# Kernel tuning notes

Hardware: AMD Instinct MI355X
Metric: run time of the kernel (lower is better)

Reference implementation:

```python
import jax, jax.numpy as jnp
import numpy as np

N_NODES = 100000
N_EDGES = 300000
N_TYPES = 3
HID = 128
EMB = 64
N_GRAPHS = 4096
T_STEPS = 4


def setup_inputs() -> dict:
    key = jax.random.key(0)
    ks = jax.random.split(key, 12)
    s = 1.0 / np.sqrt(HID)
    return {
        "node_features": jax.random.normal(ks[0], (N_NODES, HID), jnp.float32),
        "edge_index": jax.random.randint(ks[1], (N_TYPES, 2, N_EDGES), 0, N_NODES),
        "node_to_graph_id": jnp.sort(jax.random.randint(ks[2], (N_NODES,), 0, N_GRAPHS)),
        "W_msg": jax.random.normal(ks[3], (N_TYPES, HID, HID), jnp.float32) * s,
        "b_msg": jnp.zeros((N_TYPES, HID), jnp.float32),
        "W_ih": jax.random.normal(ks[4], (3 * HID, HID), jnp.float32) * s,
        "W_hh": jax.random.normal(ks[5], (3 * HID, HID), jnp.float32) * s,
        "b_ih": jnp.zeros((3 * HID,), jnp.float32),
        "b_hh": jnp.zeros((3 * HID,), jnp.float32),
        "W_proj": jax.random.normal(ks[6], (EMB, HID), jnp.float32) * s,
        "b_proj": jnp.zeros((EMB,), jnp.float32),
        "W_gate": jax.random.normal(ks[7], (EMB, HID), jnp.float32) * s,
        "b_gate": jnp.zeros((EMB,), jnp.float32),
    }


def _gru_cell(m, h, W_ih, W_hh, b_ih, b_hh):
    # torch.nn.GRUCell math; gates ordered (r, z, n)
    gi = m @ W_ih.T + b_ih          # [N, 3H]
    gh = h @ W_hh.T + b_hh          # [N, 3H]
    i_r, i_z, i_n = jnp.split(gi, 3, axis=-1)
    h_r, h_z, h_n = jnp.split(gh, 3, axis=-1)
    r = jax.nn.sigmoid(i_r + h_r)
    z = jax.nn.sigmoid(i_z + h_z)
    n = jnp.tanh(i_n + r * h_n)
    return (1.0 - z) * n + z * h


def reference(node_features, edge_index, node_to_graph_id,
              W_msg, b_msg, W_ih, W_hh, b_ih, b_hh,
              W_proj, b_proj, W_gate, b_gate):
    h = node_features  # [N, H]

    def per_type(eidx, W, b, h):
        src, dst = eidx[0], eidx[1]
        m = h[src] @ W + b  # gather + per-edge-type linear, [E, H]
        return jax.ops.segment_sum(m, dst, num_segments=N_NODES)

    for _ in range(T_STEPS):  # fixed small T: python loop is fine
        msgs = jax.vmap(per_type, in_axes=(0, 0, 0, None))(edge_index, W_msg, b_msg, h)
        m = msgs.sum(axis=0)  # [N, H] aggregated over edge types
        h = _gru_cell(m, h, W_ih, W_hh, b_ih, b_hh)

    # gated index_add graph readout (mlp_down is identity)
    proj = h @ W_proj.T + b_proj                 # [N, E]
    gate = jax.nn.sigmoid(h @ W_gate.T + b_gate)  # [N, E]
    graph_feats = jax.ops.segment_sum(gate * proj, node_to_graph_id,
                                      num_segments=N_GRAPHS)
    return graph_feats
```

## Files before the change

kernel.cpp:

```cpp
#include <hip/hip_runtime.h>
#include <hip/hip_bf16.h>
#include <math.h>

#define NN 100000
#define NNP 100096
#define NE 300000
#define HID 128
#define EMB 64
#define NG 4096
#define DEG_CAP 32
#define XS 512

typedef __bf16 bf16x8 __attribute__((ext_vector_type(8)));
typedef float  f32x16 __attribute__((ext_vector_type(16)));
typedef short  short8 __attribute__((ext_vector_type(8)));

typedef const __attribute__((address_space(1))) unsigned int* gas_u32;
typedef __attribute__((address_space(3))) unsigned int* las_u32;

__device__ __forceinline__ void gload16(const void* g, void* l) {
    __builtin_amdgcn_global_load_lds((gas_u32)g, (las_u32)l, 16, 0, 0);
}

__device__ __forceinline__ float bf2f(unsigned short u) {
    unsigned int x = ((unsigned int)u) << 16;
    return __builtin_bit_cast(float, x);
}
__device__ __forceinline__ unsigned short f2bf(float f) {
    unsigned int x = __builtin_bit_cast(unsigned int, f);
    unsigned int r = x + 0x7fff + ((x >> 16) & 1);
    return (unsigned short)(r >> 16);
}
__device__ __forceinline__ float sigm(float x) { return 1.f / (1.f + __expf(-x)); }

__global__ __launch_bounds__(256) void k_init(const float* __restrict__ nf,
                                              unsigned short* __restrict__ Y) {
    int id = blockIdx.x * 256 + threadIdx.x;
    int n = id >> 7, c = id & 127;
    Y[(long)n * HID + c] = (n < NN) ? f2bf(nf[(long)n * HID + c]) : (unsigned short)0;
}

__global__ __launch_bounds__(256) void k_build_csr(const int* __restrict__ ei,
                                                   int* __restrict__ deg,
                                                   int* __restrict__ csr) {
    int id = blockIdx.x * 256 + threadIdx.x;
    if (id >= 3 * NE) return;
    int t = id / NE;
    int i = id - t * NE;
    int src = ei[(t * 2 + 0) * NE + i];
    int dst = ei[(t * 2 + 1) * NE + i];
    int p = atomicAdd(&deg[t * NN + dst], 1);
    if (p < DEG_CAP) csr[((long)t * NN + dst) * DEG_CAP + p] = src;
}

__global__ __launch_bounds__(256) void k_pack_deg(const int* __restrict__ deg,
                                                  int4* __restrict__ degp) {
    int n = blockIdx.x * 256 + threadIdx.x;
    if (n >= NNP) return;
    int4 v; v.x = 0; v.y = 0; v.z = 0; v.w = 0;
    if (n < NN) { v.x = deg[n]; v.y = deg[NN + n]; v.z = deg[2 * NN + n]; }
    degp[n] = v;
}

__global__ __launch_bounds__(512) void k_build_w(const float* __restrict__ Wmsg,
                                                 const float* __restrict__ Wih,
                                                 const float* __restrict__ Whh,
                                                 unsigned short* __restrict__ Wnk) {
    int np = blockIdx.x;
    int k = threadIdx.x;
    int c = np >> 2, sec = np & 3;
    float v = 0.f;
    if (k < 384) {
        if (sec < 3) {
            int t = k >> 7, kk = k & 127;
            const float* wm = Wmsg + ((long)t * HID + kk) * HID;
            const float* wi = Wih + (long)(sec * HID + c) * HID;
            float s = 0.f;
            for (int j = 0; j < HID; j++) s += wm[j] * wi[j];
            v = s;
        }
    } else {
        int kk = k - 384;
        if (sec == 0)      v = Whh[(long)c * HID + kk];
        else if (sec == 1) v = Whh[(long)(HID + c) * HID + kk];
        else if (sec == 3) v = Whh[(long)(2 * HID + c) * HID + kk];
    }
    Wnk[(long)np * 512 + k] = f2bf(v);
}

__global__ __launch_bounds__(512) void k_build_bias(const float* __restrict__ bih,
                                                    const float* __restrict__ bhh,
                                                    const float* __restrict__ bmsg,
                                                    const float* __restrict__ Wih,
                                                    float* __restrict__ bbig,
                                                    float* __restrict__ Bdeg) {
    int np = threadIdx.x;
    int c = np >> 2, sec = np & 3;
    float b;
    if (sec == 0)      b = bih[c] + bhh[c];
    else if (sec == 1) b = bih[HID + c] + bhh[HID + c];
    else if (sec == 2) b = bih[2 * HID + c];
    else               b = bhh[2 * HID + c];
    bbig[np] = b;
    for (int t = 0; t < 3; t++) {
        float s = 0.f;
        if (sec < 3) {
            const float* wi = Wih + (long)(sec * HID + c) * HID;
            const float* bm = bmsg + t * HID;
            for (int j = 0; j < HID; j++) s += bm[j] * wi[j];
        }
        Bdeg[t * 512 + np] = s;
    }
}

__global__ __launch_bounds__(256) void k_agg(const unsigned short* __restrict__ Y,
                                             unsigned short* __restrict__ X,
                                             const int* __restrict__ deg,
                                             const int* __restrict__ csr) {
    const int lane = threadIdx.x & 63;
    const long n = (long)blockIdx.x * 4 + (threadIdx.x >> 6);
    const int g = lane >> 4;
    const int c16 = lane & 15;
    const int l31 = lane & 31;

    int d[3], il[3];
#pragma unroll
    for (int t = 0; t < 3; t++) {
        int dt = deg[t * NN + n];
        d[t] = dt > DEG_CAP ? DEG_CAP : dt;
        il[t] = csr[((long)t * NN + n) * DEG_CAP + l31];
    }
#pragma unroll
    for (int t = 0; t < 3; t++) {
        float acc[8] = {0.f, 0.f, 0.f, 0.f, 0.f, 0.f, 0.f, 0.f};
        int rounds = (d[t] + 3) >> 2;
        for (int r = 0; r < rounds; r++) {
            int j = r * 4 + g;
            int idx = __shfl(il[t], j & 31);
            if (j < d[t]) {
                short8 v = *(const short8*)(Y + (long)idx * HID + c16 * 8);
#pragma unroll
                for (int q = 0; q < 8; q++) acc[q] += bf2f((unsigned short)v[q]);
            }
        }
#pragma unroll
        for (int q = 0; q < 8; q++) {
            acc[q] += __shfl_xor(acc[q], 16);
            acc[q] += __shfl_xor(acc[q], 32);
        }
        if (g == 0) {
            short8 o;
#pragma unroll
            for (int q = 0; q < 8; q++) o[q] = (short)f2bf(acc[q]);
            *(short8*)(X + n * XS + t * HID + c16 * 8) = o;
        }
    }
    if (g == 1) {
        short8 v = *(const short8*)(Y + n * HID + c16 * 8);
        *(short8*)(X + n * XS + 384 + c16 * 8) = v;
    }
}

__global__ __launch_bounds__(256, 4) void k_gru_mfma(
        const unsigned short* __restrict__ X,
        const unsigned short* __restrict__ Y,
        unsigned short* __restrict__ Yw,
        const unsigned short* __restrict__ Wnk,
        const float* __restrict__ bbig, const float* __restrict__ Bdeg,
        const int4* __restrict__ degp) {
    __shared__ char lds[32768];

    const int tid = threadIdx.x;
    const int lane = tid & 63;
    const int wv = tid >> 6;
    const int wr = wv >> 1;
    const int wc = wv & 1;
    const int r31 = lane & 31;
    const int kg = lane >> 5;
    const int swr = (r31 >> 1) & 3;
    const int bn = blockIdx.x;
    const long row0 = (long)blockIdx.y * 128;

    f32x16 acc[2][2];
#pragma unroll
    for (int i = 0; i < 2; i++)
#pragma unroll
        for (int j = 0; j < 2; j++) acc[i][j] = (f32x16)(0.0f);

    const int lr = lane >> 2, su = lane & 3;
    const int r0_ = wv * 16 + lr;
    const int r1_ = 64 + wv * 16 + lr;
    const char* gA0 = (const char*)X + (row0 + r0_) * 1024 + (su ^ ((r0_ >> 1) & 3)) * 16;
    const char* gA1 = (const char*)X + (row0 + r1_) * 1024 + (su ^ ((r1_ >> 1) & 3)) * 16;
    const char* gB0 = (const char*)Wnk + (long)(bn * 128 + r0_) * 1024 + (su ^ ((r0_ >> 1) & 3)) * 16;
    const char* gB1 = (const char*)Wnk + (long)(bn * 128 + r1_) * 1024 + (su ^ ((r1_ >> 1) & 3)) * 16;
    const int dst0 = (wv * 16) * 64;
    const int dst1 = (64 + wv * 16) * 64;

    gload16(gA0, lds + dst0);
    gload16(gA1, lds + dst1);
    gload16(gB0, lds + 8192 + dst0);
    gload16(gB1, lds + 8192 + dst1);

    int cur = 0;
    for (int it = 0; it < 16; it++) {
        __syncthreads();
        if (it < 15) {
            long ko = (long)(it + 1) * 64;
            char* base = lds + (cur ^ 1) * 16384;
            gload16(gA0 + ko, base + dst0);
            gload16(gA1 + ko, base + dst1);
            gload16(gB0 + ko, base + 8192 + dst0);
            gload16(gB1 + ko, base + 8192 + dst1);
        }
        const char* Al = lds + cur * 16384;
        const char* Bl = Al + 8192;

        short8 af[2][2], bfr[2][2];
#pragma unroll
        for (int rt = 0; rt < 2; rt++)
#pragma unroll
            for (int kb = 0; kb < 2; kb++)
                af[rt][kb] = *(const short8*)(Al + (wr * 64 + rt * 32 + r31) * 64 +
                                              (((2 * kb + kg) ^ swr) * 16));
#pragma unroll
        for (int ct = 0; ct < 2; ct++)
#pragma unroll
            for (int kb = 0; kb < 2; kb++)
                bfr[ct][kb] = *(const short8*)(Bl + (wc * 64 + ct * 32 + r31) * 64 +
                                               (((2 * kb + kg) ^ swr) * 16));
#pragma unroll
        for (int kb = 0; kb < 2; kb++)
#pragma unroll
            for (int rt = 0; rt < 2; rt++)
#pragma unroll
                for (int ct = 0; ct < 2; ct++)
                    acc[rt][ct] = __builtin_amdgcn_mfma_f32_32x32x16_bf16(
                        __builtin_bit_cast(bf16x8, af[rt][kb]),
                        __builtin_bit_cast(bf16x8, bfr[ct][kb]),
                        acc[rt][ct], 0, 0, 0);
        cur ^= 1;
    }

    float* EX = (float*)lds;
#pragma unroll
    for (int band = 0; band < 4; band++) {
        __syncthreads();
        if (wr == (band >> 1)) {
            const int rt = band & 1;
#pragma unroll
            for (int ct = 0; ct < 2; ct++) {
                int col = wc * 64 + ct * 32 + r31;
#pragma unroll
                for (int q = 0; q < 16; q++) {
                    int rw = (q & 3) + 8 * (q >> 2) + 4 * kg;
                    EX[rw * 132 + col] = acc[rt][ct][q];
                }
            }
        }
        __syncthreads();
        {
            int row32 = tid >> 3, chl = tid & 7;
            long grow = row0 + band * 32 + row32;
            int4 dg = degp[grow];
            float dgx = (float)dg.x, dgy = (float)dg.y, dgz = (float)dg.z;
            ushort4 ho = *(const ushort4*)(Y + grow * HID + bn * 32 + chl * 4);
            unsigned short hold[4] = {ho.x, ho.y, ho.z, ho.w};
            ushort4 outp;
            unsigned short* op = (unsigned short*)&outp;
#pragma unroll
            for (int cc = 0; cc < 4; cc++) {
                int np = chl * 16 + cc * 4;
                float4 v  = *(const float4*)(EX + row32 * 132 + np);
                float4 bb = *(const float4*)(bbig + bn * 128 + np);
                float4 b0 = *(const float4*)(Bdeg + bn * 128 + np);
                float4 b1 = *(const float4*)(Bdeg + 512 + bn * 128 + np);
                float4 b2 = *(const float4*)(Bdeg + 1024 + bn * 128 + np);
                float Sr = v.x + bb.x + dgx * b0.x + dgy * b1.x + dgz * b2.x;
                float Sz = v.y + bb.y + dgx * b0.y + dgy * b1.y + dgz * b2.y;
                float In = v.z + bb.z + dgx * b0.z + dgy * b1.z + dgz * b2.z;
                float Hn = v.w + bb.w;
                float rr = sigm(Sr);
                float zz = sigm(Sz);
                float tt = In + rr * Hn;
                float e2 = __expf(2.f * tt);
                float nn = 1.f - 2.f / (e2 + 1.f);
                float hv = (1.f - zz) * nn + zz * bf2f(hold[cc]);
                op[cc] = f2bf(hv);
            }
            *(ushort4*)(Yw + grow * HID + bn * 32 + chl * 4) = outp;
        }
    }
}

__global__ __launch_bounds__(256) void k_readout(const unsigned short* __restrict__ Y,
                                                 const int* __restrict__ n2g,
                                                 const float* __restrict__ Wp,
                                                 const float* __restrict__ bp,
                                                 const float* __restrict__ Wg,
                                                 const float* __restrict__ bg,
                                                 float* __restrict__ out) {
    __shared__ float hs[32][132];
    __shared__ float Ws[64][129];
    int tid = threadIdx.x;
    long row0 = (long)blockIdx.x * 32;
    int rg = tid >> 5, cg = tid & 31;
    float acc[4][4];
#pragma unroll
    for (int r = 0; r < 4; r++)
#pragma unroll
        for (int c = 0; c < 4; c++) acc[r][c] = 0.f;

#pragma unroll
    for (int p = 0; p < 2; p++) {
        int e = p * 256 + tid;
        int r = e >> 4, c8 = e & 15;
        short8 v = *(const short8*)(Y + (row0 + r) * HID + c8 * 8);
#pragma unroll
        for (int j = 0; j < 8; j++) hs[r][c8 * 8 + j] = bf2f((unsigned short)v[j]);
    }
    for (int kc = 0; kc < 128; kc += 64) {
        __syncthreads();
#pragma unroll
        for (int p = 0; p < 8; p++) {
            int idx = p * 256 + tid;
            int j = idx >> 4, q = idx & 15;
            const float* Wsrc = (j < 64) ? Wp : Wg;
            float4 w = *(const float4*)&Wsrc[(j & 63) * HID + kc + q * 4];
            Ws[q * 4 + 0][j] = w.x;
            Ws[q * 4 + 1][j] = w.y;
            Ws[q * 4 + 2][j] = w.z;
            Ws[q * 4 + 3][j] = w.w;
        }
        __syncthreads();
#pragma unroll 8
        for (int k = 0; k < 64; k++) {
            float a[4], w[4];
#pragma unroll
            for (int r = 0; r < 4; r++) a[r] = hs[rg * 4 + r][kc + k];
#pragma unroll
            for (int c = 0; c < 4; c++) w[c] = Ws[k][cg + 32 * c];
#pragma unroll
            for (int r = 0; r < 4; r++)
#pragma unroll
                for (int c = 0; c < 4; c++) acc[r][c] += a[r] * w[c];
        }
    }
#pragma unroll
    for (int r = 0; r < 4; r++) {
        long row = row0 + rg * 4 + r;
        if (row < NN) {
            int g = n2g[row];
            float pv0 = acc[r][0] + bp[cg];
            float pv1 = acc[r][1] + bp[cg + 32];
            float gv0 = acc[r][2] + bg[cg];
            float gv1 = acc[r][3] + bg[cg + 32];
            atomicAdd(&out[g * EMB + cg],      pv0 * sigm(gv0));
            atomicAdd(&out[g * EMB + cg + 32], pv1 * sigm(gv1));
        }
    }
}

extern "C" void kernel_launch(void* const* d_in, const int* in_sizes, int n_in,
                              void* d_out, int out_size, void* d_ws, size_t ws_size,
                              hipStream_t stream) {
    const float* node_features = (const float*)d_in[0];
    const int*   edge_index    = (const int*)d_in[1];
    const int*   n2g           = (const int*)d_in[2];
    const float* W_msg         = (const float*)d_in[3];
    const float* b_msg         = (const float*)d_in[4];
    const float* W_ih          = (const float*)d_in[5];
    const float* W_hh          = (const float*)d_in[6];
    const float* b_ih          = (const float*)d_in[7];
    const float* b_hh          = (const float*)d_in[8];
    const float* W_proj        = (const float*)d_in[9];
    const float* b_proj        = (const float*)d_in[10];
    const float* W_gate        = (const float*)d_in[11];
    const float* b_gate        = (const float*)d_in[12];

    char* ws = (char*)d_ws;
    unsigned short* X    = (unsigned short*)(ws);
    unsigned short* Y    = (unsigned short*)(ws + 102498304);
    unsigned short* Wnk  = (unsigned short*)(ws + 128122880);
    float*          bbig = (float*)         (ws + 128647168);
    float*          Bdeg = (float*)         (ws + 128649216);
    int4*           degp = (int4*)          (ws + 128655360);
    int*            deg  = (int*)           (ws + 130256896);
    int*            csr  = (int*)           (ws + 131456896);

    float* out = (float*)d_out;

    hipMemsetAsync(out, 0, (size_t)NG * EMB * sizeof(float), stream);
    hipMemsetAsync(deg, 0, (size_t)3 * NN * sizeof(int), stream);

    k_init<<<dim3((NNP * HID) / 256), dim3(256), 0, stream>>>(node_features, Y);
    k_build_csr<<<dim3((3 * NE + 255) / 256), dim3(256), 0, stream>>>(edge_index, deg, csr);
    k_pack_deg<<<dim3(NNP / 256), dim3(256), 0, stream>>>(deg, degp);
    k_build_w<<<dim3(512), dim3(512), 0, stream>>>(W_msg, W_ih, W_hh, Wnk);
    k_build_bias<<<dim3(1), dim3(512), 0, stream>>>(b_ih, b_hh, b_msg, W_ih, bbig, Bdeg);

    for (int step = 0; step < 4; step++) {
        k_agg<<<dim3(NN / 4), dim3(256), 0, stream>>>(Y, X, deg, csr);
        k_gru_mfma<<<dim3(4, NNP / 128), dim3(256), 0, stream>>>(X, Y, Y, Wnk, bbig, Bdeg, degp);
    }
    k_readout<<<dim3(NN / 32), dim3(256), 0, stream>>>(Y, n2g, W_proj, b_proj,
                                                       W_gate, b_gate, out);
}
```

Baseline: 1.003 ms.

## Restructure GRU GEMM: full-width N per block, prepacked B fragments from global

The GRU MFMA kernel now lets each 512-thread block compute all 512 output columns for 128 rows, instead of four blocks each computing 128 columns. This stops the X tile from being reloaded four times. The weight matrix is prepacked into the MFMA fragment layout so B operands are read straight from global or L2 without LDS staging. The A tile is staged into LDS in two halves. The epilogue also writes the new hidden state into X's h-slot, so the aggregation kernel no longer copies Y into X. The cost is higher register pressure (8 accumulators per wave) and B traffic that now depends on cache hits.

```diff
diff --git a/kernel.cpp b/kernel.cpp
--- a/kernel.cpp
+++ b/kernel.cpp
@@ -34,10 +34,13 @@
 __device__ __forceinline__ float sigm(float x) { return 1.f / (1.f + __expf(-x)); }
 
 __global__ __launch_bounds__(256) void k_init(const float* __restrict__ nf,
-                                              unsigned short* __restrict__ Y) {
+                                              unsigned short* __restrict__ Y,
+                                              unsigned short* __restrict__ X) {
     int id = blockIdx.x * 256 + threadIdx.x;
     int n = id >> 7, c = id & 127;
-    Y[(long)n * HID + c] = (n < NN) ? f2bf(nf[(long)n * HID + c]) : (unsigned short)0;
+    unsigned short hv = (n < NN) ? f2bf(nf[(long)n * HID + c]) : (unsigned short)0;
+    Y[(long)n * HID + c] = hv;
+    X[(long)n * XS + 384 + c] = hv;
 }
 
 __global__ __launch_bounds__(256) void k_build_csr(const int* __restrict__ ei,
@@ -65,7 +68,7 @@
 __global__ __launch_bounds__(512) void k_build_w(const float* __restrict__ Wmsg,
                                                  const float* __restrict__ Wih,
                                                  const float* __restrict__ Whh,
-                                                 unsigned short* __restrict__ Wnk) {
+                                                 unsigned short* __restrict__ Bf) {
     int np = blockIdx.x;
     int k = threadIdx.x;
     int c = np >> 2, sec = np & 3;
@@ -85,7 +88,9 @@
         else if (sec == 1) v = Whh[(long)(HID + c) * HID + kk];
         else if (sec == 3) v = Whh[(long)(2 * HID + c) * HID + kk];
     }
-    Wnk[(long)np * 512 + k] = f2bf(v);
+    int nb = np >> 5, nl = np & 31;
+    int k16 = k >> 4, kgg = (k >> 3) & 1, e = k & 7;
+    Bf[((((nb * 32 + k16) * 2 + kgg) * 32 + nl) << 3) + e] = f2bf(v);
 }
 
 __global__ __launch_bounds__(512) void k_build_bias(const float* __restrict__ bih,
@@ -155,140 +160,135 @@
             *(short8*)(X + n * XS + t * HID + c16 * 8) = o;
         }
     }
-    if (g == 1) {
-        short8 v = *(const short8*)(Y + n * HID + c16 * 8);
-        *(short8*)(X + n * XS + 384 + c16 * 8) = v;
-    }
-}
-
-__global__ __launch_bounds__(256, 4) void k_gru_mfma(
+}
+
+__global__ __launch_bounds__(512, 2) void k_gru_mfma(
         const unsigned short* __restrict__ X,
+        unsigned short* __restrict__ Xh,
         const unsigned short* __restrict__ Y,
         unsigned short* __restrict__ Yw,
-        const unsigned short* __restrict__ Wnk,
+        const unsigned short* __restrict__ Bf,
         const float* __restrict__ bbig, const float* __restrict__ Bdeg,
         const int4* __restrict__ degp) {
-    __shared__ char lds[32768];
+    __shared__ char lds[65536];
 
     const int tid = threadIdx.x;
     const int lane = tid & 63;
     const int wv = tid >> 6;
-    const int wr = wv >> 1;
-    const int wc = wv & 1;
+    const int wr = wv >> 2;
+    const int wc = wv & 3;
     const int r31 = lane & 31;
     const int kg = lane >> 5;
-    const int swr = (r31 >> 1) & 3;
-    const int bn = blockIdx.x;
-    const long row0 = (long)blockIdx.y * 128;
-
-    f32x16 acc[2][2];
+    const long row0 = (long)blockIdx.x * 128;
+
+    f32x16 acc[2][4];
 #pragma unroll
     for (int i = 0; i < 2; i++)
 #pragma unroll
-        for (int j = 0; j < 2; j++) acc[i][j] = (f32x16)(0.0f);
-
-    const int lr = lane >> 2, su = lane & 3;
-    const int r0_ = wv * 16 + lr;
-    const int r1_ = 64 + wv * 16 + lr;
-    const char* gA0 = (const char*)X + (row0 + r0_) * 1024 + (su ^ ((r0_ >> 1) & 3)) * 16;
-    const char* gA1 = (const char*)X + (row0 + r1_) * 1024 + (su ^ ((r1_ >> 1) & 3)) * 16;
-    const char* gB0 = (const char*)Wnk + (long)(bn * 128 + r0_) * 1024 + (su ^ ((r0_ >> 1) & 3)) * 16;
-    const char* gB1 = (const char*)Wnk + (long)(bn * 128 + r1_) * 1024 + (su ^ ((r1_ >> 1) & 3)) * 16;
-    const int dst0 = (wv * 16) * 64;
-    const int dst1 = (64 + wv * 16) * 64;
-
-    gload16(gA0, lds + dst0);
-    gload16(gA1, lds + dst1);
-    gload16(gB0, lds + 8192 + dst0);
-    gload16(gB1, lds + 8192 + dst1);
-
-    int cur = 0;
+        for (int j = 0; j < 4; j++) acc[i][j] = (f32x16)(0.0f);
+
+    const char* pA = (const char*)X + (row0 + lane) * 1024;
+#define STAGE_A(H)                                                              \
+    {                                                                           \
+        _Pragma("unroll")                                                       \
+        for (int jj = 0; jj < 8; jj++) {                                        \
+            gload16(pA + ((jj & 1) * 65536 + (H) * 512 +                        \
+                          (wv * 2 + (jj >> 2)) * 32 + ((jj >> 1) & 1) * 16),    \
+                    lds + (wv * 8 + jj) * 1024);                                \
+        }                                                                       \
+    }
+
+    const unsigned short* pB0 = Bf + (wc * 4 + 0) * 16384 + lane * 8;
+    const unsigned short* pB1 = Bf + (wc * 4 + 1) * 16384 + lane * 8;
+    const unsigned short* pB2 = Bf + (wc * 4 + 2) * 16384 + lane * 8;
+    const unsigned short* pB3 = Bf + (wc * 4 + 3) * 16384 + lane * 8;
+
+    const int vAoff = kg * 2048 + wr * 1024 + r31 * 16;
+    const char* ldsA = lds;
+
+    STAGE_A(0);
+    __syncthreads();
+
+#pragma unroll
     for (int it = 0; it < 16; it++) {
+        if (it == 8) {
+            __syncthreads();
+            STAGE_A(1);
+            __syncthreads();
+        }
+#pragma unroll
+        for (int kb = 0; kb < 2; kb++) {
+            const int kl = (it & 7) * 2 + kb;
+            const int k16 = it * 2 + kb;
+            short8 af0 = *(const short8*)(ldsA + kl * 4096 + vAoff);
+            short8 af1 = *(const short8*)(ldsA + kl * 4096 + 512 + vAoff);
+            short8 b0 = *(const short8*)(pB0 + k16 * 512);
+            short8 b1 = *(const short8*)(pB1 + k16 * 512);
+            short8 b2 = *(const short8*)(pB2 + k16 * 512);
+            short8 b3 = *(const short8*)(pB3 + k16 * 512);
+            acc[0][0] = __builtin_amdgcn_mfma_f32_32x32x16_bf16(
+                __builtin_bit_cast(bf16x8, af0), __builtin_bit_cast(bf16x8, b0), acc[0][0], 0, 0, 0);
+            acc[0][1] = __builtin_amdgcn_mfma_f32_32x32x16_bf16(
+                __builtin_bit_cast(bf16x8, af0), __builtin_bit_cast(bf16x8, b1), acc[0][1], 0, 0, 0);
+            acc[0][2] = __builtin_amdgcn_mfma_f32_32x32x16_bf16(
+                __builtin_bit_cast(bf16x8, af0), __builtin_bit_cast(bf16x8, b2), acc[0][2], 0, 0, 0);
+            acc[0][3] = __builtin_amdgcn_mfma_f32_32x32x16_bf16(
+                __builtin_bit_cast(bf16x8, af0), __builtin_bit_cast(bf16x8, b3), acc[0][3], 0, 0, 0);
+            acc[1][0] = __builtin_amdgcn_mfma_f32_32x32x16_bf16(
+                __builtin_bit_cast(bf16x8, af1), __builtin_bit_cast(bf16x8, b0), acc[1][0], 0, 0, 0);
+            acc[1][1] = __builtin_amdgcn_mfma_f32_32x32x16_bf16(
+                __builtin_bit_cast(bf16x8, af1), __builtin_bit_cast(bf16x8, b1), acc[1][1], 0, 0, 0);
+            acc[1][2] = __builtin_amdgcn_mfma_f32_32x32x16_bf16(
+                __builtin_bit_cast(bf16x8, af1), __builtin_bit_cast(bf16x8, b2), acc[1][2], 0, 0, 0);
+            acc[1][3] = __builtin_amdgcn_mfma_f32_32x32x16_bf16(
+                __builtin_bit_cast(bf16x8, af1), __builtin_bit_cast(bf16x8, b3), acc[1][3], 0, 0, 0);
+        }
+    }
+
+    float* EX = (float*)lds;
+    const int ch = tid & 127;
+    const int rbase = tid >> 7;
+    const float4 bb = *(const float4*)(bbig + ch * 4);
+    const float4 e0 = *(const float4*)(Bdeg + ch * 4);
+    const float4 e1 = *(const float4*)(Bdeg + 512 + ch * 4);
+    const float4 e2 = *(const float4*)(Bdeg + 1024 + ch * 4);
+
+#pragma unroll
+    for (int b = 0; b < 4; b++) {
         __syncthreads();
-        if (it < 15) {
-            long ko = (long)(it + 1) * 64;
-            char* base = lds + (cur ^ 1) * 16384;
-            gload16(gA0 + ko, base + dst0);
-            gload16(gA1 + ko, base + dst1);
-            gload16(gB0 + ko, base + 8192 + dst0);
-            gload16(gB1 + ko, base + 8192 + dst1);
-        }
-        const char* Al = lds + cur * 16384;
-        const char* Bl = Al + 8192;
-
-        short8 af[2][2], bfr[2][2];
-#pragma unroll
-        for (int rt = 0; rt < 2; rt++)
-#pragma unroll
-            for (int kb = 0; kb < 2; kb++)
-                af[rt][kb] = *(const short8*)(Al + (wr * 64 + rt * 32 + r31) * 64 +
-                                              (((2 * kb + kg) ^ swr) * 16));
-#pragma unroll
-        for (int ct = 0; ct < 2; ct++)
-#pragma unroll
-            for (int kb = 0; kb < 2; kb++)
-                bfr[ct][kb] = *(const short8*)(Bl + (wc * 64 + ct * 32 + r31) * 64 +
-                                               (((2 * kb + kg) ^ swr) * 16));
-#pragma unroll
-        for (int kb = 0; kb < 2; kb++)
-#pragma unroll
-            for (int rt = 0; rt < 2; rt++)
-#pragma unroll
-                for (int ct = 0; ct < 2; ct++)
-                    acc[rt][ct] = __builtin_amdgcn_mfma_f32_32x32x16_bf16(
-                        __builtin_bit_cast(bf16x8, af[rt][kb]),
-                        __builtin_bit_cast(bf16x8, bfr[ct][kb]),
-                        acc[rt][ct], 0, 0, 0);
-        cur ^= 1;
-    }
-
-    float* EX = (float*)lds;
-#pragma unroll
-    for (int band = 0; band < 4; band++) {
-        __syncthreads();
-        if (wr == (band >> 1)) {
-            const int rt = band & 1;
-#pragma unroll
-            for (int ct = 0; ct < 2; ct++) {
-                int col = wc * 64 + ct * 32 + r31;
+        if (wr == (b >> 1)) {
+            const int rt = b & 1;
+#pragma unroll
+            for (int ct = 0; ct < 4; ct++) {
+                int col = wc * 128 + ct * 32 + r31;
 #pragma unroll
                 for (int q = 0; q < 16; q++) {
                     int rw = (q & 3) + 8 * (q >> 2) + 4 * kg;
-                    EX[rw * 132 + col] = acc[rt][ct][q];
+                    EX[rw * 512 + col] = acc[rt][ct][q];
                 }
             }
         }
         __syncthreads();
-        {
-            int row32 = tid >> 3, chl = tid & 7;
-            long grow = row0 + band * 32 + row32;
+#pragma unroll
+        for (int i = 0; i < 8; i++) {
+            int rw = rbase + 4 * i;
+            long grow = row0 + b * 32 + rw;
             int4 dg = degp[grow];
             float dgx = (float)dg.x, dgy = (float)dg.y, dgz = (float)dg.z;
-            ushort4 ho = *(const ushort4*)(Y + grow * HID + bn * 32 + chl * 4);
-            unsigned short hold[4] = {ho.x, ho.y, ho.z, ho.w};
-            ushort4 outp;
-            unsigned short* op = (unsigned short*)&outp;
-#pragma unroll
-            for (int cc = 0; cc < 4; cc++) {
-                int np = chl * 16 + cc * 4;
-                float4 v  = *(const float4*)(EX + row32 * 132 + np);
-                float4 bb = *(const float4*)(bbig + bn * 128 + np);
-                float4 b0 = *(const float4*)(Bdeg + bn * 128 + np);
-                float4 b1 = *(const float4*)(Bdeg + 512 + bn * 128 + np);
-                float4 b2 = *(const float4*)(Bdeg + 1024 + bn * 128 + np);
-                float Sr = v.x + bb.x + dgx * b0.x + dgy * b1.x + dgz * b2.x;
-                float Sz = v.y + bb.y + dgx * b0.y + dgy * b1.y + dgz * b2.y;
-                float In = v.z + bb.z + dgx * b0.z + dgy * b1.z + dgz * b2.z;
-                float Hn = v.w + bb.w;
-                float rr = sigm(Sr);
-                float zz = sigm(Sz);
-                float tt = In + rr * Hn;
-                float e2 = __expf(2.f * tt);
-                float nn = 1.f - 2.f / (e2 + 1.f);
-                float hv = (1.f - zz) * nn + zz * bf2f(hold[cc]);
-                op[cc] = f2bf(hv);
-            }
-            *(ushort4*)(Yw + grow * HID + bn * 32 + chl * 4) = outp;
+            float4 v = *(const float4*)(EX + rw * 512 + ch * 4);
+            float Sr = v.x + bb.x + dgx * e0.x + dgy * e1.x + dgz * e2.x;
+            float Sz = v.y + bb.y + dgx * e0.y + dgy * e1.y + dgz * e2.y;
+            float In = v.z + bb.z + dgx * e0.z + dgy * e1.z + dgz * e2.z;
+            float Hn = v.w + bb.w;
+            float rr = sigm(Sr);
+            float zz = sigm(Sz);
+            float tt = In + rr * Hn;
+            float ee = __expf(2.f * tt);
+            float nn = 1.f - 2.f / (ee + 1.f);
+            float hv = (1.f - zz) * nn + zz * bf2f(Y[grow * HID + ch]);
+            unsigned short hb = f2bf(hv);
+            Yw[grow * HID + ch] = hb;
+            Xh[grow * XS + 384 + ch] = hb;
         }
     }
 }
@@ -381,7 +381,7 @@
     char* ws = (char*)d_ws;
     unsigned short* X    = (unsigned short*)(ws);
     unsigned short* Y    = (unsigned short*)(ws + 102498304);
-    unsigned short* Wnk  = (unsigned short*)(ws + 128122880);
+    unsigned short* Bf   = (unsigned short*)(ws + 128122880);
     float*          bbig = (float*)         (ws + 128647168);
     float*          Bdeg = (float*)         (ws + 128649216);
     int4*           degp = (int4*)          (ws + 128655360);
@@ -393,15 +393,16 @@
     hipMemsetAsync(out, 0, (size_t)NG * EMB * sizeof(float), stream);
     hipMemsetAsync(deg, 0, (size_t)3 * NN * sizeof(int), stream);
 
-    k_init<<<dim3((NNP * HID) / 256), dim3(256), 0, stream>>>(node_features, Y);
+    k_init<<<dim3((NNP * HID) / 256), dim3(256), 0, stream>>>(node_features, Y, X);
     k_build_csr<<<dim3((3 * NE + 255) / 256), dim3(256), 0, stream>>>(edge_index, deg, csr);
     k_pack_deg<<<dim3(NNP / 256), dim3(256), 0, stream>>>(deg, degp);
-    k_build_w<<<dim3(512), dim3(512), 0, stream>>>(W_msg, W_ih, W_hh, Wnk);
+    k_build_w<<<dim3(512), dim3(512), 0, stream>>>(W_msg, W_ih, W_hh, Bf);
     k_build_bias<<<dim3(1), dim3(512), 0, stream>>>(b_ih, b_hh, b_msg, W_ih, bbig, Bdeg);
 
     for (int step = 0; step < 4; step++) {
         k_agg<<<dim3(NN / 4), dim3(256), 0, stream>>>(Y, X, deg, csr);
-        k_gru_mfma<<<dim3(4, NNP / 128), dim3(256), 0, stream>>>(X, Y, Y, Wnk, bbig, Bdeg, degp);
+        k_gru_mfma<<<dim3(NNP / 128), dim3(512), 0, stream>>>(X, X, Y, Y, Bf,
+                                                              bbig, Bdeg, degp);
     }
     k_readout<<<dim3(NN / 32), dim3(256), 0, stream>>>(Y, n2g, W_proj, b_proj,
                                                        W_gate, b_gate, out);
```

New measurement: 928.3 us. 7.5% less time.
